# Kernel optimization log

Hardware: AMD Instinct MI355X
Metric: run time of the kernel (lower is better)

## Reference

```python
import jax, jax.numpy as jnp
import numpy as np

B, L, D, A, N, E, V, C = 16, 2048, 256, 128, 256, 50000, 30522, 128
H = D // 2  # GRU hidden per direction
EPS = 1e-5


def _rn(k, shape, s=0.02):
    return jax.random.normal(k, shape, jnp.float32) * s


def setup_inputs() -> dict:
    ks = jax.random.split(jax.random.key(0), 24)
    z = lambda *s: jnp.zeros(s, jnp.float32)
    return {
        "x": jax.random.randint(ks[0], (B, L), 0, V),
        "attention_mask": jnp.ones((B, L), jnp.float32),
        "nodes": jax.random.randint(ks[1], (B, N), 0, E),
        "node_mask": jnp.ones((B, N), jnp.float32),
        "D_D": jax.random.uniform(ks[2], (A, A), jnp.float32),
        "D_F": jax.random.uniform(ks[3], (B, A, N), jnp.float32),
        "word_embed": _rn(ks[4], (V, D)),
        "label_embed": _rn(ks[5], (A, D)),
        "entity_embed": _rn(ks[6], (E, D)),
        "W1": _rn(ks[7], (D, D)), "W2": _rn(ks[8], (D, D)),
        "W3": _rn(ks[9], (D, D)), "W4": _rn(ks[10], (D, D)),
        "W6_w": _rn(ks[11], (D, 2 * D)), "W6_b": z(D),
        "V1": _rn(ks[12], (D,), 1.0), "V2": _rn(ks[13], (D,), 1.0),
        "gru_wih_f": _rn(ks[14], (3 * H, D)), "gru_whh_f": _rn(ks[15], (3 * H, H)),
        "gru_bih_f": z(3 * H), "gru_bhh_f": z(3 * H),
        "gru_wih_b": _rn(ks[16], (3 * H, D)), "gru_whh_b": _rn(ks[17], (3 * H, H)),
        "gru_bih_b": z(3 * H), "gru_bhh_b": z(3 * H),
        "conv1_w": _rn(ks[18], (D, D, 3)), "conv1_b": z(D),
        "conv2_w": _rn(ks[19], (D, D, 4)), "conv2_b": z(D),
        "conv3_w": _rn(ks[20], (D, D, 5)), "conv3_b": z(D),
        "cls1_w": _rn(ks[21], (1024, 2 * D)), "cls1_b": z(1024),
        "cls2_w": _rn(ks[22], (C, 1024)), "cls2_b": z(C),
    }


def _gru_dir(x, wih, whh, bih, bhh, reverse):
    # x: [B,L,d] -> outputs [B,L,H]; torch GRU cell math
    gi = jnp.swapaxes(x, 0, 1) @ wih.T + bih  # [L,B,3H], input proj precomputed
    h0 = jnp.zeros((x.shape[0], whh.shape[1]), x.dtype)

    def step(h, g):
        gh = h @ whh.T + bhh
        ir, iz, inn = jnp.split(g, 3, -1)
        hr, hz, hn = jnp.split(gh, 3, -1)
        r = jax.nn.sigmoid(ir + hr)
        zt = jax.nn.sigmoid(iz + hz)
        n = jnp.tanh(inn + r * hn)
        hnew = (1.0 - zt) * n + zt * h
        return hnew, hnew

    _, hs = jax.lax.scan(step, h0, gi, reverse=reverse)
    return jnp.swapaxes(hs, 0, 1)


def _conv1d(x, w, b):
    # x: [B,C,L], w: [O,I,K], VALID padding (torch Conv1d default)
    y = jax.lax.conv_general_dilated(x, w, (1,), "VALID",
                                     dimension_numbers=("NCH", "OIH", "NCH"))
    return y + b[None, :, None]


def reference(x, attention_mask, nodes, node_mask, D_D, D_F, word_embed, label_embed,
              entity_embed, W1, W2, W3, W4, W6_w, W6_b, V1, V2,
              gru_wih_f, gru_whh_f, gru_bih_f, gru_bhh_f,
              gru_wih_b, gru_whh_b, gru_bih_b, gru_bhh_b,
              conv1_w, conv1_b, conv2_w, conv2_b, conv3_w, conv3_b,
              cls1_w, cls1_b, cls2_w, cls2_b):
    Dm = label_embed                                  # [A,d]
    Fm = entity_embed[nodes] * node_mask[..., None]   # [B,N,d]
    D_hat = jax.nn.relu(
        Dm @ W1.T
        + (D_D @ (Dm @ W2.T)) / (jnp.sum(D_D, 1, keepdims=True) + EPS)
        + (D_D.T @ (Dm @ W3.T)) / (jnp.sum(D_D.T, 1, keepdims=True) + EPS)
    )                                                 # [A,d]
    F_hat = jax.nn.relu(
        Fm @ W4.T
        + jnp.einsum("ban,ad->bnd", D_F, D_hat) / (jnp.sum(D_F, 1)[..., None] + EPS)
    ) * node_mask[..., None]                          # [B,N,d]

    xe = word_embed[x]                                # [B,L,d]
    hf = _gru_dir(xe, gru_wih_f, gru_whh_f, gru_bih_f, gru_bhh_f, False)
    hb = _gru_dir(xe, gru_wih_b, gru_whh_b, gru_bih_b, gru_bhh_b, True)
    H1 = jnp.mean(jnp.concatenate([hf, hb], -1), axis=1)  # [B,d]

    def attn_pool(feats, ctx, Vvec):
        cat = jnp.concatenate([feats, jnp.broadcast_to(ctx[:, None, :], feats.shape)], -1)
        U = jnp.tanh(cat @ W6_w.T + W6_b)             # [B,n,d]
        alpha = jax.nn.softmax(jnp.einsum("bnd,d->bn", U, Vvec), axis=1)
        return jnp.einsum("bn,bnd->bd", alpha, U)

    Hf = attn_pool(F_hat, H1, V1)                     # [B,d]
    xt = jnp.swapaxes(xe, 1, 2)                       # [B,d,L]
    Y = jnp.concatenate([
        jnp.swapaxes(_conv1d(xt, conv1_w, conv1_b), 1, 2),
        jnp.swapaxes(_conv1d(xt, conv2_w, conv2_b), 1, 2),
        jnp.swapaxes(_conv1d(xt, conv3_w, conv3_b), 1, 2),
    ], axis=1)                                        # [B,3L-12+3,d]
    Ht = attn_pool(Y, Hf, V2)                         # [B,d]
    Hcat = jnp.concatenate([Hf, Ht], -1)              # [B,2d]
    return jax.nn.relu(Hcat @ cls1_w.T + cls1_b) @ cls2_w.T + cls2_b
```

## Files before the change

kernel.cpp:

```cpp
#include <hip/hip_runtime.h>
#include <cstdint>
#include <cstddef>

constexpr int kB = 16, kL = 2048, kD = 256, kA = 128, kN = 256, kC = 128;
constexpr int kH = 128, kG = 384, kGN = 768;
constexpr int kT1 = 2046, kT2 = 2045, kT3 = 2044, kTT = 6135;
constexpr float kEPS = 1e-5f;

constexpr int kCTile = 48;
constexpr int kCBlkPerSeg = 43 * kB;
constexpr int kConvBlocks = 3 * kCBlkPerSeg;
constexpr int kGruBlocks = 32;

constexpr size_t OFF_XE   = 0;
constexpr size_t OFF_GI   = OFF_XE + (size_t)kB*kL*kD;
constexpr size_t OFF_FHAT = OFF_GI + (size_t)kB*kL*kGN;
constexpr size_t OFF_UF   = OFF_FHAT + (size_t)kB*kN*kD;
constexpr size_t OFF_EFFW = OFF_UF + (size_t)kB*kN*kD;
constexpr size_t OFF_EFFB = OFF_EFFW + (size_t)12*kD*kD;
constexpr size_t OFF_W6AT = OFF_EFFB + (size_t)3*kD;
constexpr size_t OFF_W6BT = OFF_W6AT + (size_t)kD*kD;
constexpr size_t OFF_W1T  = OFF_W6BT + (size_t)kD*kD;
constexpr size_t OFF_W2T  = OFF_W1T + (size_t)kD*kD;
constexpr size_t OFF_W3T  = OFF_W2T + (size_t)kD*kD;
constexpr size_t OFF_W4T  = OFF_W3T + (size_t)kD*kD;
constexpr size_t OFF_DHAT = OFF_W4T + (size_t)kD*kD;
constexpr size_t OFF_P1   = OFF_DHAT + (size_t)kA*kD;
constexpr size_t OFF_P2   = OFF_P1 + (size_t)kA*kD;
constexpr size_t OFF_P3   = OFF_P2 + (size_t)kA*kD;
constexpr size_t OFF_RS   = OFF_P3 + (size_t)kA*kD;
constexpr size_t OFF_CS   = OFF_RS + kA;
constexpr size_t OFF_H1   = OFF_CS + kA;
constexpr size_t OFF_C1   = OFF_H1 + (size_t)kB*kD;
constexpr size_t OFF_HFv  = OFF_C1 + (size_t)kB*kD;
constexpr size_t OFF_C2   = OFF_HFv + (size_t)kB*kD;
constexpr size_t OFF_HT   = OFF_C2 + (size_t)kB*kD;
constexpr size_t OFF_SCF  = OFF_HT + (size_t)kB*kD;
constexpr size_t OFF_SC   = OFF_SCF + (size_t)kB*kN;
constexpr size_t OFF_PART = OFF_SC + (size_t)kB*kTT;
constexpr size_t OFF_PBUF = OFF_PART + (size_t)48*kB*kD;
constexpr size_t TOTAL_CONCURRENT = OFF_PBUF + (size_t)kB*kTT*kD;

__device__ __forceinline__ float sigm(float x) { return 1.f / (1.f + __expf(-x)); }
__device__ __forceinline__ float tanh_fast(float x) {
  x = fminf(15.f, fmaxf(-15.f, x));
  float e2 = __expf(2.f * x);
  return (e2 - 1.f) / (e2 + 1.f);
}

__global__ void k_transpose(float* dst, const float* src, int stride) {
  int i = blockIdx.x, d = threadIdx.x;
  dst[i * kD + d] = src[(size_t)d * stride + i];
}

__global__ void k_rowcol(const float* DDm, float* rs, float* cs) {
  int a = threadIdx.x;
  float r = 0.f, c = 0.f;
  for (int j = 0; j < kA; ++j) { r += DDm[a * kA + j]; c += DDm[j * kA + a]; }
  rs[a] = r; cs[a] = c;
}

__global__ void k_proj3(const float* Dm, const float* W1T, const float* W2T, const float* W3T,
                        float* P1, float* P2, float* P3) {
  __shared__ float row[kD];
  int a = blockIdx.x, d = threadIdx.x;
  row[d] = Dm[a * kD + d];
  __syncthreads();
  float s1 = 0, s2 = 0, s3 = 0;
  for (int i = 0; i < kD; ++i) {
    float v = row[i];
    s1 = fmaf(v, W1T[i * kD + d], s1);
    s2 = fmaf(v, W2T[i * kD + d], s2);
    s3 = fmaf(v, W3T[i * kD + d], s3);
  }
  P1[a * kD + d] = s1; P2[a * kD + d] = s2; P3[a * kD + d] = s3;
}

__global__ void k_dhat(const float* DDm, const float* P1, const float* P2, const float* P3,
                       const float* rs, const float* cs, float* Dhat) {
  __shared__ float drow[kA], dcol[kA];
  int a = blockIdx.x, d = threadIdx.x;
  if (d < kA) { drow[d] = DDm[a * kA + d]; dcol[d] = DDm[d * kA + a]; }
  __syncthreads();
  float q2 = 0, q3 = 0;
  for (int j = 0; j < kA; ++j) {
    q2 = fmaf(drow[j], P2[j * kD + d], q2);
    q3 = fmaf(dcol[j], P3[j * kD + d], q3);
  }
  float v = P1[a * kD + d] + q2 / (rs[a] + kEPS) + q3 / (cs[a] + kEPS);
  Dhat[a * kD + d] = v > 0.f ? v : 0.f;
}

__global__ void k_fhat(const int* nodes, const float* nmask, const float* eemb,
                       const float* DF, const float* W4T, const float* Dhat, float* Fhat) {
  int b = blockIdx.y, n0 = blockIdx.x * 16, d = threadIdx.x;
  __shared__ float fm[16][kD];
  __shared__ float dc[kA][16];
  __shared__ float den[16], msk[16];
  for (int r = 0; r < 16; ++r) {
    int idx = nodes[b * kN + n0 + r];
    float m = nmask[b * kN + n0 + r];
    fm[r][d] = eemb[(size_t)idx * kD + d] * m;
    if (d == 0) msk[r] = m;
  }
  for (int q = 0; q < 8; ++q) {
    int e = q * 256 + d;
    int aa = e >> 4, nn = e & 15;
    dc[aa][nn] = DF[(size_t)b * kA * kN + (size_t)aa * kN + n0 + nn];
  }
  __syncthreads();
  if (d < 16) {
    float s = 0.f;
    for (int aa = 0; aa < kA; ++aa) s += dc[aa][d];
    den[d] = s;
  }
  __syncthreads();
  float a1[16], a2[16];
#pragma unroll
  for (int n = 0; n < 16; ++n) { a1[n] = 0.f; a2[n] = 0.f; }
  for (int i = 0; i < kD; ++i) {
    float w = W4T[i * kD + d];
#pragma unroll
    for (int n = 0; n < 16; ++n) a1[n] = fmaf(fm[n][i], w, a1[n]);
  }
  for (int aa = 0; aa < kA; ++aa) {
    float w = Dhat[aa * kD + d];
#pragma unroll
    for (int n = 0; n < 16; ++n) a2[n] = fmaf(dc[aa][n], w, a2[n]);
  }
#pragma unroll
  for (int n = 0; n < 16; ++n) {
    float v = a1[n] + a2[n] / (den[n] + kEPS);
    v = v > 0.f ? v : 0.f;
    Fhat[((size_t)b * kN + n0 + n) * kD + d] = v * msk[n];
  }
}

__global__ void k_xe(const int* x, const float* wemb, float* xe) {
  int r0 = blockIdx.x * 16;
  int t = threadIdx.x;
  int rr = t >> 6, c = t & 63;
  for (int s = 0; s < 4; ++s) {
    int r = r0 + rr + s * 4;
    int idx = x[r];
    ((float4*)(xe + (size_t)r * kD))[c] = ((const float4*)(wemb + (size_t)idx * kD))[c];
  }
}

__global__ __launch_bounds__(256) void k_gemm_gi(const float* Aa, const float* wf, const float* wb,
                                                 const float* bf, const float* bb, float* Cc) {
  __shared__ alignas(16) float As[64][68];
  __shared__ alignas(16) float Bs[64][68];
  int m0 = blockIdx.x * 64, n0 = blockIdx.y * 64;
  int tid = threadIdx.x;
  int tx = tid & 15, ty = tid >> 4;
  float acc[4][4];
#pragma unroll
  for (int q = 0; q < 4; ++q)
#pragma unroll
    for (int p = 0; p < 4; ++p) acc[q][p] = 0.f;
  for (int kk = 0; kk < 256; kk += 64) {
    {
      int r = tid >> 2, c0 = (tid & 3) * 16;
      const float* src = Aa + (size_t)(m0 + r) * kD + kk + c0;
      float4 v0 = ((const float4*)src)[0], v1 = ((const float4*)src)[1];
      float4 v2 = ((const float4*)src)[2], v3 = ((const float4*)src)[3];
      *((float4*)&As[r][c0])      = v0; *((float4*)&As[r][c0 + 4])  = v1;
      *((float4*)&As[r][c0 + 8])  = v2; *((float4*)&As[r][c0 + 12]) = v3;
      int n = n0 + r;
      const float* wsrc = (n < kG) ? (wf + (size_t)n * kD) : (wb + (size_t)(n - kG) * kD);
      wsrc += kk + c0;
      float4 w0 = ((const float4*)wsrc)[0], w1 = ((const float4*)wsrc)[1];
      float4 w2 = ((const float4*)wsrc)[2], w3 = ((const float4*)wsrc)[3];
      *((float4*)&Bs[r][c0])      = w0; *((float4*)&Bs[r][c0 + 4])  = w1;
      *((float4*)&Bs[r][c0 + 8])  = w2; *((float4*)&Bs[r][c0 + 12]) = w3;
    }
    __syncthreads();
#pragma unroll 4
    for (int k4 = 0; k4 < 16; ++k4) {
      float4 av[4], bv[4];
#pragma unroll
      for (int q = 0; q < 4; ++q) av[q] = *(const float4*)&As[ty * 4 + q][k4 * 4];
#pragma unroll
      for (int p = 0; p < 4; ++p) bv[p] = *(const float4*)&Bs[tx * 4 + p][k4 * 4];
#pragma unroll
      for (int q = 0; q < 4; ++q)
#pragma unroll
        for (int p = 0; p < 4; ++p) {
          acc[q][p] = fmaf(av[q].x, bv[p].x, acc[q][p]);
          acc[q][p] = fmaf(av[q].y, bv[p].y, acc[q][p]);
          acc[q][p] = fmaf(av[q].z, bv[p].z, acc[q][p]);
          acc[q][p] = fmaf(av[q].w, bv[p].w, acc[q][p]);
        }
    }
    __syncthreads();
  }
  int nbase = n0 + tx * 4;
  float bb4[4];
#pragma unroll
  for (int p = 0; p < 4; ++p) {
    int n = nbase + p;
    bb4[p] = (n < kG) ? bf[n] : bb[n - kG];
  }
#pragma unroll
  for (int q = 0; q < 4; ++q) {
    int m = m0 + ty * 4 + q;
    float4 o = make_float4(acc[q][0] + bb4[0], acc[q][1] + bb4[1],
                           acc[q][2] + bb4[2], acc[q][3] + bb4[3]);
    *((float4*)(Cc + (size_t)m * kGN + nbase)) = o;
  }
}

__device__ __forceinline__ int hpad(int i) { return (i >> 5) * 36 + (i & 31); }

__global__ __launch_bounds__(768, 3) void k_main(
    const float* __restrict__ gi, const float* __restrict__ whh_f, const float* __restrict__ whh_b,
    const float* __restrict__ bhh_f, const float* __restrict__ bhh_b, float* __restrict__ H1,
    const float* __restrict__ xe, const float* __restrict__ effW, const float* __restrict__ effB,
    float* __restrict__ P, int idOffset) {
  __shared__ alignas(16) float smem[(kCTile + 4) * kD];
  int id = blockIdx.x + idOffset;
  int tid = threadIdx.x;

  if (id < kGruBlocks) {
    int b = id >> 1, dir = id & 1;
    const float* whh = dir ? whh_b : whh_f;
    const float* bhh = dir ? bhh_b : bhh_f;
    float* h_sh = smem;
    float* gh   = smem + 144;

    int s = tid & 3;
    int g = tid >> 2;
    float w[2][32];
#pragma unroll
    for (int q = 0; q < 2; ++q) {
      const float4* wp = (const float4*)(whh + (size_t)(g * 2 + q) * kH + s * 32);
#pragma unroll
      for (int r = 0; r < 8; ++r) {
        float4 v = wp[r];
        w[q][4 * r] = v.x; w[q][4 * r + 1] = v.y; w[q][4 * r + 2] = v.z; w[q][4 * r + 3] = v.w;
      }
    }
    for (int i = tid; i < 144; i += 768) h_sh[i] = 0.f;

    float hreg = 0.f, hsum = 0.f;
    float bhr = 0.f, bhz = 0.f, bhn = 0.f;
    float ar = 0.f, az = 0.f, an = 0.f;
    float br = 0.f, bz = 0.f, bn = 0.f;
    const float* gib = gi + (size_t)b * kL * kGN + dir * kG + tid;
    if (tid < kH) {
      bhr = bhh[tid]; bhz = bhh[tid + kH]; bhn = bhh[tid + 2 * kH];
      const float* r0 = gib + (size_t)(dir ? (kL - 1) : 0) * kGN;
      const float* r1 = gib + (size_t)(dir ? (kL - 2) : 1) * kGN;
      ar = r0[0]; az = r0[kH]; an = r0[2 * kH];
      br = r1[0]; bz = r1[kH]; bn = r1[2 * kH];
    }
    __syncthreads();

#define GRU_STEP(cr, cz, cn, T)                                                   \
    {                                                                             \
      const float* hp = h_sh + s * 36;                                            \
      float4 h0 = *(const float4*)(hp + 0),  h1 = *(const float4*)(hp + 4);       \
      float4 h2 = *(const float4*)(hp + 8),  h3 = *(const float4*)(hp + 12);      \
      float4 h4 = *(const float4*)(hp + 16), h5 = *(const float4*)(hp + 20);      \
      float4 h6 = *(const float4*)(hp + 24), h7 = *(const float4*)(hp + 28);      \
      float a0 = 0.f, a1 = 0.f;                                                   \
      const float4 hv[8] = {h0, h1, h2, h3, h4, h5, h6, h7};                      \
      _Pragma("unroll")                                                           \
      for (int r = 0; r < 8; ++r) {                                               \
        float4 hh = hv[r];                                                        \
        a0 = fmaf(hh.x, w[0][4 * r], a0);     a1 = fmaf(hh.x, w[1][4 * r], a1);   \
        a0 = fmaf(hh.y, w[0][4 * r + 1], a0); a1 = fmaf(hh.y, w[1][4 * r + 1], a1);\
        a0 = fmaf(hh.z, w[0][4 * r + 2], a0); a1 = fmaf(hh.z, w[1][4 * r + 2], a1);\
        a0 = fmaf(hh.w, w[0][4 * r + 3], a0); a1 = fmaf(hh.w, w[1][4 * r + 3], a1);\
      }                                                                           \
      a0 += __shfl_xor(a0, 1); a0 += __shfl_xor(a0, 2);                           \
      a1 += __shfl_xor(a1, 1); a1 += __shfl_xor(a1, 2);                           \
      if (s == 0) { float2 o = make_float2(a0, a1); *(float2*)(gh + g * 2) = o; } \
      __syncthreads();                                                            \
      if (tid < kH) {                                                             \
        int tn = (T) + 2; if (tn > kL - 1) tn = kL - 1;                           \
        const float* gq = gib + (size_t)(dir ? (kL - 1 - tn) : tn) * kGN;         \
        float lr = gq[0], lz = gq[kH], ln = gq[2 * kH];                           \
        float hr = gh[tid] + bhr;                                                 \
        float hz = gh[tid + kH] + bhz;                                            \
        float hn = gh[tid + 2 * kH] + bhn;                                        \
        float rg = sigm(cr + hr);                                                 \
        float zg = sigm(cz + hz);                                                 \
        float ng = tanh_fast(cn + rg * hn);                                       \
        hreg = (1.f - zg) * ng + zg * hreg;                                       \
        hsum += hreg;                                                             \
        h_sh[hpad(tid)] = hreg;                                                   \
        cr = lr; cz = lz; cn = ln;                                                \
      }                                                                           \
      __syncthreads();                                                            \
    }

    for (int t = 0; t < kL; t += 2) {
      GRU_STEP(ar, az, an, t)
      GRU_STEP(br, bz, bn, t + 1)
    }
#undef GRU_STEP
    if (tid < kH) H1[b * kD + dir * kH + tid] = hsum * (1.f / (float)kL);

  } else {
    int cid = id - kGruBlocks;
    int seg = cid / kCBlkPerSeg;
    int rem = cid - seg * kCBlkPerSeg;
    int b = rem / 43;
    int tb = rem - b * 43;
    int t0 = tb * kCTile;
    int K = 3 + seg;
    int tapbase = (seg == 0) ? 0 : (seg == 1) ? 3 : 7;
    int Toff = (seg == 0) ? 0 : (seg == 1) ? kT1 : (kT1 + kT2);
    int Tk = (seg == 0) ? kT1 : (seg == 1) ? kT2 : kT3;

    float (*xl)[kD] = (float(*)[kD])smem;
    int nrow = kCTile + K - 1;
    {
      int total4 = nrow * 64;
      for (int gq = tid; gq < total4; gq += 768) {
        int r = gq >> 6, c4 = gq & 63;
        int row = t0 + r; if (row > kL - 1) row = kL - 1;
        ((float4*)&xl[r][0])[c4] = ((const float4*)(xe + ((size_t)b * kL + row) * kD))[c4];
      }
    }
    __syncthreads();

    int tx = tid & 63, tg = tid >> 6;
    int d0 = tx * 4;
    float acc[4][4];
#pragma unroll
    for (int tt = 0; tt < 4; ++tt)
#pragma unroll
      for (int q = 0; q < 4; ++q) acc[tt][q] = 0.f;
    for (int tap = 0; tap < K; ++tap) {
      const float* wq = effW + (size_t)(tapbase + tap) * kD * kD + d0;
      int rbase = tg * 4 + tap;
#pragma unroll 2
      for (int i = 0; i < kD; i += 4) {
        float4 xv[4];
#pragma unroll
        for (int tt = 0; tt < 4; ++tt) xv[tt] = *(const float4*)&xl[rbase + tt][i];
#pragma unroll
        for (int c = 0; c < 4; ++c) {
          float4 w4 = *(const float4*)(wq + (size_t)(i + c) * kD);
#pragma unroll
          for (int tt = 0; tt < 4; ++tt) {
            float xc = (c == 0) ? xv[tt].x : (c == 1) ? xv[tt].y : (c == 2) ? xv[tt].z : xv[tt].w;
            acc[tt][0] = fmaf(xc, w4.x, acc[tt][0]);
            acc[tt][1] = fmaf(xc, w4.y, acc[tt][1]);
            acc[tt][2] = fmaf(xc, w4.z, acc[tt][2]);
            acc[tt][3] = fmaf(xc, w4.w, acc[tt][3]);
          }
        }
      }
    }
    float4 eb = *(const float4*)(effB + seg * kD + d0);
#pragma unroll
    for (int tt = 0; tt < 4; ++tt) {
      int t = t0 + tg * 4 + tt;
      if (t < Tk) {
        float4 o = make_float4(acc[tt][0] + eb.x, acc[tt][1] + eb.y,
                               acc[tt][2] + eb.z, acc[tt][3] + eb.w);
        *((float4*)(P + ((size_t)b * kTT + Toff + t) * kD + d0)) = o;
      }
    }
  }
}

__global__ void k_ctxproj(const float* vec, const float* W6bT, const float* w6bias, float* out) {
  __shared__ float vrow[kD];
  int b = blockIdx.x, d = threadIdx.x;
  vrow[d] = vec[b * kD + d];
  __syncthreads();
  float acc = w6bias[d];
  for (int i = 0; i < kD; ++i) acc = fmaf(vrow[i], W6bT[i * kD + d], acc);
  out[b * kD + d] = acc;
}

__global__ void k_attn1(const float* Fhat, const float* W6aT, const float* c1,
                        const float* V1, float* UF, float* scF) {
  int b = blockIdx.y, n0 = blockIdx.x * 16, d = threadIdx.x;
  __shared__ float fr[16][kD];
  __shared__ float red[16][8];
  for (int r = 0; r < 16; ++r) fr[r][d] = Fhat[((size_t)b * kN + n0 + r) * kD + d];
  __syncthreads();
  float u[16];
#pragma unroll
  for (int n = 0; n < 16; ++n) u[n] = 0.f;
  for (int i = 0; i < kD; ++i) {
    float w = W6aT[i * kD + d];
#pragma unroll
    for (int n = 0; n < 16; ++n) u[n] = fmaf(fr[n][i], w, u[n]);
  }
  float cb = c1[b * kD + d];
  float v1 = V1[d];
  int lane = d & 63, wv = d >> 6;
#pragma unroll
  for (int n = 0; n < 16; ++n) {
    float uu = tanh_fast(u[n] + cb);
    UF[((size_t)b * kN + n0 + n) * kD + d] = uu;
    float p = uu * v1;
    p += __shfl_xor(p, 1); p += __shfl_xor(p, 2); p += __shfl_xor(p, 4);
    p += __shfl_xor(p, 8); p += __shfl_xor(p, 16); p += __shfl_xor(p, 32);
    if (lane == 0) red[n][wv] = p;
  }
  __syncthreads();
  if (d < 16) scF[b * kN + n0 + d] = red[d][0] + red[d][1] + red[d][2] + red[d][3];
}

__global__ void k_attn1_fin(const float* scF, const float* UF, float* Hf) {
  int b = blockIdx.x, d = threadIdx.x;
  __shared__ float al[kN];
  __shared__ float red[4];
  float sv = scF[b * kN + d];
  float m = sv;
#pragma unroll
  for (int o = 1; o < 64; o <<= 1) m = fmaxf(m, __shfl_xor(m, o));
  if ((d & 63) == 0) red[d >> 6] = m;
  __syncthreads();
  float mm = fmaxf(fmaxf(red[0], red[1]), fmaxf(red[2], red[3]));
  float e = __expf(sv - mm);
  float s = e;
#pragma unroll
  for (int o = 1; o < 64; o <<= 1) s += __shfl_xor(s, o);
  __syncthreads();
  if ((d & 63) == 0) red[d >> 6] = s;
  __syncthreads();
  float tot = red[0] + red[1] + red[2] + red[3];
  al[d] = e / tot;
  __syncthreads();
  float acc = 0.f;
  for (int n = 0; n < kN; ++n) acc = fmaf(al[n], UF[((size_t)b * kN + n) * kD + d], acc);
  Hf[b * kD + d] = acc;
}

__global__ void k_fold(const float* cw1, const float* cw2, const float* cw3,
                       const float* W6aT, float* effW) {
  int tapg = blockIdx.y, i0 = blockIdx.x * 4, d = threadIdx.x;
  const float* cw; int K, tap;
  if (tapg < 3)      { cw = cw1; K = 3; tap = tapg; }
  else if (tapg < 7) { cw = cw2; K = 4; tap = tapg - 3; }
  else               { cw = cw3; K = 5; tap = tapg - 7; }
  __shared__ float cc[4][kD];
#pragma unroll
  for (int ii = 0; ii < 4; ++ii)
    cc[ii][d] = cw[((size_t)d * kD + (i0 + ii)) * K + tap];
  __syncthreads();
  float acc[4] = {0.f, 0.f, 0.f, 0.f};
  for (int jj = 0; jj < kD; ++jj) {
    float w = W6aT[jj * kD + d];
#pragma unroll
    for (int ii = 0; ii < 4; ++ii) acc[ii] = fmaf(cc[ii][jj], w, acc[ii]);
  }
#pragma unroll
  for (int ii = 0; ii < 4; ++ii)
    effW[((size_t)tapg * kD + i0 + ii) * kD + d] = acc[ii];
}

__global__ void k_effb(const float* b1, const float* b2, const float* b3,
                       const float* W6aT, float* effB) {
  int c = blockIdx.x, d = threadIdx.x;
  const float* bb = (c == 0) ? b1 : ((c == 1) ? b2 : b3);
  __shared__ float bl[kD];
  bl[d] = bb[d];
  __syncthreads();
  float acc = 0.f;
  for (int j = 0; j < kD; ++j) acc = fmaf(bl[j], W6aT[j * kD + d], acc);
  effB[c * kD + d] = acc;
}

__global__ void k_score(const float* P, const float* c2, const float* V2, float* sc) {
  int b = blockIdx.y;
  int t0 = blockIdx.x * 32;
  int tid = threadIdx.x;
  int w = tid >> 6, lane = tid & 63;
  float4 c2v = ((const float4*)(c2 + (size_t)b * kD))[lane];
  float4 v2v = ((const float4*)V2)[lane];
#pragma unroll
  for (int it = 0; it < 8; ++it) {
    int t = t0 + it * 4 + w;
    if (t < kTT) {
      float4 p = ((const float4*)(P + ((size_t)b * kTT + t) * kD))[lane];
      float s = tanh_fast(p.x + c2v.x) * v2v.x + tanh_fast(p.y + c2v.y) * v2v.y +
                tanh_fast(p.z + c2v.z) * v2v.z + tanh_fast(p.w + c2v.w) * v2v.w;
      s += __shfl_xor(s, 1); s += __shfl_xor(s, 2); s += __shfl_xor(s, 4);
      s += __shfl_xor(s, 8); s += __shfl_xor(s, 16); s += __shfl_xor(s, 32);
      if (lane == 0) sc[(size_t)b * kTT + t] = s;
    }
  }
}

__global__ void k_sm2(float* sc) {
  int b = blockIdx.x, tid = threadIdx.x;
  __shared__ float red[4];
  float m = -1e30f;
  for (int t = tid; t < kTT; t += 256) m = fmaxf(m, sc[(size_t)b * kTT + t]);
#pragma unroll
  for (int o = 1; o < 64; o <<= 1) m = fmaxf(m, __shfl_xor(m, o));
  if ((tid & 63) == 0) red[tid >> 6] = m;
  __syncthreads();
  float mm = fmaxf(fmaxf(red[0], red[1]), fmaxf(red[2], red[3]));
  float s = 0.f;
  for (int t = tid; t < kTT; t += 256) s += __expf(sc[(size_t)b * kTT + t] - mm);
#pragma unroll
  for (int o = 1; o < 64; o <<= 1) s += __shfl_xor(s, o);
  __syncthreads();
  if ((tid & 63) == 0) red[tid >> 6] = s;
  __syncthreads();
  float inv = 1.f / (red[0] + red[1] + red[2] + red[3]);
  for (int t = tid; t < kTT; t += 256) sc[(size_t)b * kTT + t] = __expf(sc[(size_t)b * kTT + t] - mm) * inv;
}

__global__ void k_aws(const float* sc, const float* P, const float* c2, float* part) {
  int cchunk = blockIdx.x, b = blockIdx.y, d = threadIdx.x;
  int tbeg = cchunk * 128;
  int tend = tbeg + 128; if (tend > kTT) tend = kTT;
  float c2d = c2[(size_t)b * kD + d];
  float acc = 0.f;
  for (int t = tbeg; t < tend; ++t)
    acc = fmaf(sc[(size_t)b * kTT + t], tanh_fast(P[((size_t)b * kTT + t) * kD + d] + c2d), acc);
  part[((size_t)cchunk * kB + b) * kD + d] = acc;
}

__global__ void k_ared(const float* part, float* Ht) {
  int b = blockIdx.x, d = threadIdx.x;
  float acc = 0.f;
  for (int cc = 0; cc < 48; ++cc) acc += part[((size_t)cc * kB + b) * kD + d];
  Ht[b * kD + d] = acc;
}

__global__ __launch_bounds__(1024) void k_cls(const float* Hf, const float* Ht,
                                              const float* w1, const float* b1,
                                              const float* w2, const float* b2, float* out) {
  int b = blockIdx.x, tid = threadIdx.x;
  __shared__ alignas(16) float hc[2 * kD];
  __shared__ alignas(16) float act[1024];
  if (tid < kD) hc[tid] = Hf[b * kD + tid];
  else if (tid < 2 * kD) hc[tid] = Ht[b * kD + tid - kD];
  __syncthreads();
  {
    float acc = b1[tid];
    const float4* wr = (const float4*)(w1 + (size_t)tid * 2 * kD);
    const float4* hr = (const float4*)hc;
    for (int i = 0; i < 128; ++i) {
      float4 wv = wr[i]; float4 hv = hr[i];
      acc += wv.x * hv.x + wv.y * hv.y + wv.z * hv.z + wv.w * hv.w;
    }
    act[tid] = acc > 0.f ? acc : 0.f;
  }
  __syncthreads();
  if (tid < kC) {
    float acc = b2[tid];
    const float4* wr = (const float4*)(w2 + (size_t)tid * 1024);
    const float4* ar = (const float4*)act;
    for (int i = 0; i < 256; ++i) {
      float4 wv = wr[i]; float4 av = ar[i];
      acc += wv.x * av.x + wv.y * av.y + wv.z * av.z + wv.w * av.w;
    }
    out[b * kC + tid] = acc;
  }
}

extern "C" void kernel_launch(void* const* d_in, const int* in_sizes, int n_in,
                              void* d_out, int out_size, void* d_ws, size_t ws_size,
                              hipStream_t stream) {
  (void)in_sizes; (void)n_in; (void)out_size;
  const int*   x     = (const int*)d_in[0];
  const int*   nodes = (const int*)d_in[2];
  const float* nmask = (const float*)d_in[3];
  const float* DDm   = (const float*)d_in[4];
  const float* DF    = (const float*)d_in[5];
  const float* wemb  = (const float*)d_in[6];
  const float* lemb  = (const float*)d_in[7];
  const float* eemb  = (const float*)d_in[8];
  const float* W1    = (const float*)d_in[9];
  const float* W2    = (const float*)d_in[10];
  const float* W3    = (const float*)d_in[11];
  const float* W4    = (const float*)d_in[12];
  const float* W6w   = (const float*)d_in[13];
  const float* W6bia = (const float*)d_in[14];
  const float* V1v   = (const float*)d_in[15];
  const float* V2v   = (const float*)d_in[16];
  const float* wih_f = (const float*)d_in[17];
  const float* whh_f = (const float*)d_in[18];
  const float* bih_f = (const float*)d_in[19];
  const float* bhh_f = (const float*)d_in[20];
  const float* wih_b = (const float*)d_in[21];
  const float* whh_b = (const float*)d_in[22];
  const float* bih_b = (const float*)d_in[23];
  const float* bhh_b = (const float*)d_in[24];
  const float* c1w   = (const float*)d_in[25];
  const float* c1b   = (const float*)d_in[26];
  const float* c2w   = (const float*)d_in[27];
  const float* c2b   = (const float*)d_in[28];
  const float* c3w   = (const float*)d_in[29];
  const float* c3b   = (const float*)d_in[30];
  const float* cls1w = (const float*)d_in[31];
  const float* cls1b = (const float*)d_in[32];
  const float* cls2w = (const float*)d_in[33];
  const float* cls2b = (const float*)d_in[34];
  float* out = (float*)d_out;
  float* ws  = (float*)d_ws;

  float* xe   = ws + OFF_XE;
  float* gi   = ws + OFF_GI;
  float* Fhat = ws + OFF_FHAT;
  float* UF   = ws + OFF_UF;
  float* effW = ws + OFF_EFFW;
  float* effB = ws + OFF_EFFB;
  float* w6at = ws + OFF_W6AT;
  float* w6bt = ws + OFF_W6BT;
  float* w1t  = ws + OFF_W1T;
  float* w2t  = ws + OFF_W2T;
  float* w3t  = ws + OFF_W3T;
  float* w4t  = ws + OFF_W4T;
  float* dhat = ws + OFF_DHAT;
  float* p1   = ws + OFF_P1;
  float* p2   = ws + OFF_P2;
  float* p3   = ws + OFF_P3;
  float* rs   = ws + OFF_RS;
  float* cs   = ws + OFF_CS;
  float* H1b  = ws + OFF_H1;
  float* c1bf = ws + OFF_C1;
  float* Hfb  = ws + OFF_HFv;
  float* c2bf = ws + OFF_C2;
  float* Htb  = ws + OFF_HT;
  float* scF  = ws + OFF_SCF;
  float* sc   = ws + OFF_SC;
  float* part = ws + OFF_PART;

  bool concurrent = ws_size >= TOTAL_CONCURRENT * sizeof(float);
  float* Pbuf = concurrent ? (ws + OFF_PBUF) : gi;

  k_xe<<<2048, 256, 0, stream>>>(x, wemb, xe);
  k_transpose<<<kD, kD, 0, stream>>>(w1t, W1, kD);
  k_transpose<<<kD, kD, 0, stream>>>(w2t, W2, kD);
  k_transpose<<<kD, kD, 0, stream>>>(w3t, W3, kD);
  k_transpose<<<kD, kD, 0, stream>>>(w4t, W4, kD);
  k_transpose<<<kD, kD, 0, stream>>>(w6at, W6w, 2 * kD);
  k_transpose<<<kD, kD, 0, stream>>>(w6bt, W6w + kD, 2 * kD);
  k_gemm_gi<<<dim3(512, 12), 256, 0, stream>>>(xe, wih_f, wih_b, bih_f, bih_b, gi);

  k_rowcol<<<1, kA, 0, stream>>>(DDm, rs, cs);
  k_proj3<<<kA, kD, 0, stream>>>(lemb, w1t, w2t, w3t, p1, p2, p3);
  k_dhat<<<kA, kD, 0, stream>>>(DDm, p1, p2, p3, rs, cs, dhat);
  k_fhat<<<dim3(16, kB), kD, 0, stream>>>(nodes, nmask, eemb, DF, w4t, dhat, Fhat);

  k_fold<<<dim3(64, 12), kD, 0, stream>>>(c1w, c2w, c3w, w6at, effW);
  k_effb<<<3, kD, 0, stream>>>(c1b, c2b, c3b, w6at, effB);

  if (concurrent) {
    k_main<<<kGruBlocks + kConvBlocks, 768, 0, stream>>>(
        gi, whh_f, whh_b, bhh_f, bhh_b, H1b, xe, effW, effB, Pbuf, 0);
  } else {
    k_main<<<kGruBlocks, 768, 0, stream>>>(
        gi, whh_f, whh_b, bhh_f, bhh_b, H1b, xe, effW, effB, Pbuf, 0);
    k_main<<<kConvBlocks, 768, 0, stream>>>(
        gi, whh_f, whh_b, bhh_f, bhh_b, H1b, xe, effW, effB, Pbuf, kGruBlocks);
  }

  k_ctxproj<<<kB, kD, 0, stream>>>(H1b, w6bt, W6bia, c1bf);
  k_attn1<<<dim3(16, kB), kD, 0, stream>>>(Fhat, w6at, c1bf, V1v, UF, scF);
  k_attn1_fin<<<kB, kD, 0, stream>>>(scF, UF, Hfb);
  k_ctxproj<<<kB, kD, 0, stream>>>(Hfb, w6bt, W6bia, c2bf);

  k_score<<<dim3(192, kB), 256, 0, stream>>>(Pbuf, c2bf, V2v, sc);
  k_sm2<<<kB, 256, 0, stream>>>(sc);
  k_aws<<<dim3(48, kB), kD, 0, stream>>>(sc, Pbuf, c2bf, part);
  k_ared<<<kB, kD, 0, stream>>>(part, Htb);
  k_cls<<<kB, 1024, 0, stream>>>(Hfb, Htb, cls1w, cls1b, cls2w, cls2b, out);
}
```

Measured before the change: 2.197 ms.

## Restructure GRU recurrence to 1024 threads with one barrier per step

The GRU recurrence in the fused main kernel now runs with 1024 threads. Each group of 8 lanes owns one hidden unit and computes all three gate dot products, reducing them with DPP lane swizzles instead of shuffles. The kernel double-buffers h in shared memory so each step needs a single barrier rather than two, and input-projection rows for 8 future steps are staged into shared memory in chunks instead of loaded per step. The conv path is adapted to 1024 threads with 3 time rows per thread group. This targets the serial latency per GRU step, at the cost of more threads per block and different register and occupancy pressure in the conv blocks.

```diff
diff --git a/kernel.cpp b/kernel.cpp
--- a/kernel.cpp
+++ b/kernel.cpp
@@ -11,6 +11,10 @@
 constexpr int kCBlkPerSeg = 43 * kB;
 constexpr int kConvBlocks = 3 * kCBlkPerSeg;
 constexpr int kGruBlocks = 32;
+
+constexpr int kSmemFloats = 21504;
+
+typedef float f32x4 __attribute__((ext_vector_type(4)));
 
 constexpr size_t OFF_XE   = 0;
 constexpr size_t OFF_GI   = OFF_XE + (size_t)kB*kL*kD;
@@ -48,6 +52,19 @@
   return (e2 - 1.f) / (e2 + 1.f);
 }
 
+__device__ __forceinline__ float dpp_xor1(float x) {
+  int r = __builtin_amdgcn_update_dpp(0, __builtin_bit_cast(int, x), 0xB1, 0xF, 0xF, true);
+  return __builtin_bit_cast(float, r);
+}
+__device__ __forceinline__ float dpp_xor2(float x) {
+  int r = __builtin_amdgcn_update_dpp(0, __builtin_bit_cast(int, x), 0x4E, 0xF, 0xF, true);
+  return __builtin_bit_cast(float, r);
+}
+__device__ __forceinline__ float dpp_mirr8(float x) {
+  int r = __builtin_amdgcn_update_dpp(0, __builtin_bit_cast(int, x), 0x141, 0xF, 0xF, true);
+  return __builtin_bit_cast(float, r);
+}
+
 __global__ void k_transpose(float* dst, const float* src, int stride) {
   int i = blockIdx.x, d = threadIdx.x;
   dst[i * kD + d] = src[(size_t)d * stride + i];
@@ -211,14 +228,15 @@
   }
 }
 
-__device__ __forceinline__ int hpad(int i) { return (i >> 5) * 36 + (i & 31); }
-
-__global__ __launch_bounds__(768, 3) void k_main(
+__global__
+__attribute__((amdgpu_flat_work_group_size(1024, 1024)))
+__attribute__((amdgpu_waves_per_eu(4, 4)))
+void k_main(
     const float* __restrict__ gi, const float* __restrict__ whh_f, const float* __restrict__ whh_b,
     const float* __restrict__ bhh_f, const float* __restrict__ bhh_b, float* __restrict__ H1,
     const float* __restrict__ xe, const float* __restrict__ effW, const float* __restrict__ effB,
     float* __restrict__ P, int idOffset) {
-  __shared__ alignas(16) float smem[(kCTile + 4) * kD];
+  __shared__ alignas(16) float smem[kSmemFloats];
   int id = blockIdx.x + idOffset;
   int tid = threadIdx.x;
 
@@ -226,82 +244,83 @@
     int b = id >> 1, dir = id & 1;
     const float* whh = dir ? whh_b : whh_f;
     const float* bhh = dir ? bhh_b : bhh_f;
-    float* h_sh = smem;
-    float* gh   = smem + 144;
-
-    int s = tid & 3;
-    int g = tid >> 2;
-    float w[2][32];
-#pragma unroll
-    for (int q = 0; q < 2; ++q) {
-      const float4* wp = (const float4*)(whh + (size_t)(g * 2 + q) * kH + s * 32);
-#pragma unroll
-      for (int r = 0; r < 8; ++r) {
-        float4 v = wp[r];
-        w[q][4 * r] = v.x; w[q][4 * r + 1] = v.y; w[q][4 * r + 2] = v.z; w[q][4 * r + 3] = v.w;
-      }
-    }
-    for (int i = tid; i < 144; i += 768) h_sh[i] = 0.f;
-
-    float hreg = 0.f, hsum = 0.f;
-    float bhr = 0.f, bhz = 0.f, bhn = 0.f;
-    float ar = 0.f, az = 0.f, an = 0.f;
-    float br = 0.f, bz = 0.f, bn = 0.f;
-    const float* gib = gi + (size_t)b * kL * kGN + dir * kG + tid;
-    if (tid < kH) {
-      bhr = bhh[tid]; bhz = bhh[tid + kH]; bhn = bhh[tid + 2 * kH];
-      const float* r0 = gib + (size_t)(dir ? (kL - 1) : 0) * kGN;
-      const float* r1 = gib + (size_t)(dir ? (kL - 2) : 1) * kGN;
-      ar = r0[0]; az = r0[kH]; an = r0[2 * kH];
-      br = r1[0]; bz = r1[kH]; bn = r1[2 * kH];
-    }
+    float* hb = smem;
+    float* gt = smem + 320;
+
+    int i = tid >> 3, q = tid & 7;
+    int hpad_i = i + ((i >> 4) << 2);
+
+    const f32x4* wrp = (const f32x4*)(whh + (size_t)i * kH + q * 16);
+    const f32x4* wzp = (const f32x4*)(whh + (size_t)(kH + i) * kH + q * 16);
+    const f32x4* wnp = (const f32x4*)(whh + (size_t)(2 * kH + i) * kH + q * 16);
+    f32x4 wr0 = wrp[0], wr1 = wrp[1], wr2 = wrp[2], wr3 = wrp[3];
+    f32x4 wz0 = wzp[0], wz1 = wzp[1], wz2 = wzp[2], wz3 = wzp[3];
+    f32x4 wn0 = wnp[0], wn1 = wnp[1], wn2 = wnp[2], wn3 = wnp[3];
+
+    float bhr = bhh[i], bhz = bhh[kH + i], bhn = bhh[2 * kH + i];
+
+    const float* gibase = gi + (size_t)b * kL * kGN + dir * kG;
+    float va, vb, vc;
+
+#define STAGE_LOAD(T)                                                          \
+    { int o0 = tid / 384, c0 = tid - o0 * 384;                                 \
+      int r0 = dir ? (kL - 1 - ((T) + o0)) : ((T) + o0);                       \
+      r0 = r0 < 0 ? 0 : (r0 > kL - 1 ? kL - 1 : r0);                           \
+      va = gibase[(size_t)r0 * kGN + c0];                                      \
+      int u1 = tid + 1024; int o1 = u1 / 384, c1 = u1 - o1 * 384;              \
+      int r1 = dir ? (kL - 1 - ((T) + o1)) : ((T) + o1);                       \
+      r1 = r1 < 0 ? 0 : (r1 > kL - 1 ? kL - 1 : r1);                           \
+      vb = gibase[(size_t)r1 * kGN + c1];                                      \
+      int u2 = tid + 2048; int o2 = u2 / 384, c2 = u2 - o2 * 384;              \
+      int r2 = dir ? (kL - 1 - ((T) + o2)) : ((T) + o2);                       \
+      r2 = r2 < 0 ? 0 : (r2 > kL - 1 ? kL - 1 : r2);                           \
+      vc = gibase[(size_t)r2 * kGN + c2]; }
+
+#define STAGE_WRITE(cbuf)                                                      \
+    { gt[(cbuf) * 3072 + tid] = va;                                            \
+      gt[(cbuf) * 3072 + tid + 1024] = vb;                                     \
+      gt[(cbuf) * 3072 + tid + 2048] = vc; }
+
+    for (int u = tid; u < 320; u += 1024) hb[u] = 0.f;
+    STAGE_LOAD(0)
+    STAGE_WRITE(0)
+    float hprev = 0.f, hsum = 0.f;
     __syncthreads();
 
-#define GRU_STEP(cr, cz, cn, T)                                                   \
-    {                                                                             \
-      const float* hp = h_sh + s * 36;                                            \
-      float4 h0 = *(const float4*)(hp + 0),  h1 = *(const float4*)(hp + 4);       \
-      float4 h2 = *(const float4*)(hp + 8),  h3 = *(const float4*)(hp + 12);      \
-      float4 h4 = *(const float4*)(hp + 16), h5 = *(const float4*)(hp + 20);      \
-      float4 h6 = *(const float4*)(hp + 24), h7 = *(const float4*)(hp + 28);      \
-      float a0 = 0.f, a1 = 0.f;                                                   \
-      const float4 hv[8] = {h0, h1, h2, h3, h4, h5, h6, h7};                      \
-      _Pragma("unroll")                                                           \
-      for (int r = 0; r < 8; ++r) {                                               \
-        float4 hh = hv[r];                                                        \
-        a0 = fmaf(hh.x, w[0][4 * r], a0);     a1 = fmaf(hh.x, w[1][4 * r], a1);   \
-        a0 = fmaf(hh.y, w[0][4 * r + 1], a0); a1 = fmaf(hh.y, w[1][4 * r + 1], a1);\
-        a0 = fmaf(hh.z, w[0][4 * r + 2], a0); a1 = fmaf(hh.z, w[1][4 * r + 2], a1);\
-        a0 = fmaf(hh.w, w[0][4 * r + 3], a0); a1 = fmaf(hh.w, w[1][4 * r + 3], a1);\
-      }                                                                           \
-      a0 += __shfl_xor(a0, 1); a0 += __shfl_xor(a0, 2);                           \
-      a1 += __shfl_xor(a1, 1); a1 += __shfl_xor(a1, 2);                           \
-      if (s == 0) { float2 o = make_float2(a0, a1); *(float2*)(gh + g * 2) = o; } \
-      __syncthreads();                                                            \
-      if (tid < kH) {                                                             \
-        int tn = (T) + 2; if (tn > kL - 1) tn = kL - 1;                           \
-        const float* gq = gib + (size_t)(dir ? (kL - 1 - tn) : tn) * kGN;         \
-        float lr = gq[0], lz = gq[kH], ln = gq[2 * kH];                           \
-        float hr = gh[tid] + bhr;                                                 \
-        float hz = gh[tid + kH] + bhz;                                            \
-        float hn = gh[tid + 2 * kH] + bhn;                                        \
-        float rg = sigm(cr + hr);                                                 \
-        float zg = sigm(cz + hz);                                                 \
-        float ng = tanh_fast(cn + rg * hn);                                       \
-        hreg = (1.f - zg) * ng + zg * hreg;                                       \
-        hsum += hreg;                                                             \
-        h_sh[hpad(tid)] = hreg;                                                   \
-        cr = lr; cz = lz; cn = ln;                                                \
-      }                                                                           \
-      __syncthreads();                                                            \
-    }
-
-    for (int t = 0; t < kL; t += 2) {
-      GRU_STEP(ar, az, an, t)
-      GRU_STEP(br, bz, bn, t + 1)
-    }
-#undef GRU_STEP
-    if (tid < kH) H1[b * kD + dir * kH + tid] = hsum * (1.f / (float)kL);
+#define FMA_Q(hq, wrq, wzq, wnq)                                               \
+    ar = fmaf(hq.x, wrq.x, ar); az = fmaf(hq.x, wzq.x, az); an = fmaf(hq.x, wnq.x, an); \
+    ar = fmaf(hq.y, wrq.y, ar); az = fmaf(hq.y, wzq.y, az); an = fmaf(hq.y, wnq.y, an); \
+    ar = fmaf(hq.z, wrq.z, ar); az = fmaf(hq.z, wzq.z, az); an = fmaf(hq.z, wnq.z, an); \
+    ar = fmaf(hq.w, wrq.w, ar); az = fmaf(hq.w, wzq.w, az); an = fmaf(hq.w, wnq.w, an);
+
+    for (int t = 0; t < kL; ++t) {
+      int cb = (t >> 3) & 1;
+      if ((t & 7) == 0 && t + 8 < kL) STAGE_LOAD(t + 8)
+      const f32x4* hp = (const f32x4*)(hb + (t & 1) * 160 + q * 20);
+      f32x4 h0 = hp[0], h1 = hp[1], h2 = hp[2], h3 = hp[3];
+      float ar = 0.f, az = 0.f, an = 0.f;
+      FMA_Q(h0, wr0, wz0, wn0)
+      FMA_Q(h1, wr1, wz1, wn1)
+      FMA_Q(h2, wr2, wz2, wn2)
+      FMA_Q(h3, wr3, wz3, wn3)
+      ar += dpp_xor1(ar); az += dpp_xor1(az); an += dpp_xor1(an);
+      ar += dpp_xor2(ar); az += dpp_xor2(az); an += dpp_xor2(an);
+      ar += dpp_mirr8(ar); az += dpp_mirr8(az); an += dpp_mirr8(an);
+      int gb = cb * 3072 + (t & 7) * 384 + i;
+      float gir = gt[gb], giz = gt[gb + kH], gin = gt[gb + 2 * kH];
+      float rr = sigm(gir + ar + bhr);
+      float zz = sigm(giz + az + bhz);
+      float nn = tanh_fast(gin + rr * (an + bhn));
+      hprev = (1.f - zz) * nn + zz * hprev;
+      hsum += hprev;
+      if (q == 0) hb[((t + 1) & 1) * 160 + hpad_i] = hprev;
+      if ((t & 7) == 7 && t + 1 < kL) STAGE_WRITE(cb ^ 1)
+      __syncthreads();
+    }
+#undef FMA_Q
+#undef STAGE_LOAD
+#undef STAGE_WRITE
+    if (q == 0) H1[b * kD + dir * kH + i] = hsum * (1.f / (float)kL);
 
   } else {
     int cid = id - kGruBlocks;
@@ -319,7 +338,7 @@
     int nrow = kCTile + K - 1;
     {
       int total4 = nrow * 64;
-      for (int gq = tid; gq < total4; gq += 768) {
+      for (int gq = tid; gq < total4; gq += 1024) {
         int r = gq >> 6, c4 = gq & 63;
         int row = t0 + r; if (row > kL - 1) row = kL - 1;
         ((float4*)&xl[r][0])[c4] = ((const float4*)(xe + ((size_t)b * kL + row) * kD))[c4];
@@ -329,24 +348,24 @@
 
     int tx = tid & 63, tg = tid >> 6;
     int d0 = tx * 4;
-    float acc[4][4];
-#pragma unroll
-    for (int tt = 0; tt < 4; ++tt)
-#pragma unroll
-      for (int q = 0; q < 4; ++q) acc[tt][q] = 0.f;
+    float acc[3][4];
+#pragma unroll
+    for (int tt = 0; tt < 3; ++tt)
+#pragma unroll
+      for (int qq = 0; qq < 4; ++qq) acc[tt][qq] = 0.f;
     for (int tap = 0; tap < K; ++tap) {
       const float* wq = effW + (size_t)(tapbase + tap) * kD * kD + d0;
-      int rbase = tg * 4 + tap;
+      int rbase = tg * 3 + tap;
 #pragma unroll 2
-      for (int i = 0; i < kD; i += 4) {
-        float4 xv[4];
-#pragma unroll
-        for (int tt = 0; tt < 4; ++tt) xv[tt] = *(const float4*)&xl[rbase + tt][i];
+      for (int ii = 0; ii < kD; ii += 4) {
+        float4 xv[3];
+#pragma unroll
+        for (int tt = 0; tt < 3; ++tt) xv[tt] = *(const float4*)&xl[rbase + tt][ii];
 #pragma unroll
         for (int c = 0; c < 4; ++c) {
-          float4 w4 = *(const float4*)(wq + (size_t)(i + c) * kD);
-#pragma unroll
-          for (int tt = 0; tt < 4; ++tt) {
+          float4 w4 = *(const float4*)(wq + (size_t)(ii + c) * kD);
+#pragma unroll
+          for (int tt = 0; tt < 3; ++tt) {
             float xc = (c == 0) ? xv[tt].x : (c == 1) ? xv[tt].y : (c == 2) ? xv[tt].z : xv[tt].w;
             acc[tt][0] = fmaf(xc, w4.x, acc[tt][0]);
             acc[tt][1] = fmaf(xc, w4.y, acc[tt][1]);
@@ -358,8 +377,8 @@
     }
     float4 eb = *(const float4*)(effB + seg * kD + d0);
 #pragma unroll
-    for (int tt = 0; tt < 4; ++tt) {
-      int t = t0 + tg * 4 + tt;
+    for (int tt = 0; tt < 3; ++tt) {
+      int t = t0 + tg * 3 + tt;
       if (t < Tk) {
         float4 o = make_float4(acc[tt][0] + eb.x, acc[tt][1] + eb.y,
                                acc[tt][2] + eb.z, acc[tt][3] + eb.w);
@@ -652,12 +671,12 @@
   k_effb<<<3, kD, 0, stream>>>(c1b, c2b, c3b, w6at, effB);
 
   if (concurrent) {
-    k_main<<<kGruBlocks + kConvBlocks, 768, 0, stream>>>(
+    k_main<<<kGruBlocks + kConvBlocks, 1024, 0, stream>>>(
         gi, whh_f, whh_b, bhh_f, bhh_b, H1b, xe, effW, effB, Pbuf, 0);
   } else {
-    k_main<<<kGruBlocks, 768, 0, stream>>>(
+    k_main<<<kGruBlocks, 1024, 0, stream>>>(
         gi, whh_f, whh_b, bhh_f, bhh_b, H1b, xe, effW, effB, Pbuf, 0);
-    k_main<<<kConvBlocks, 768, 0, stream>>>(
+    k_main<<<kConvBlocks, 1024, 0, stream>>>(
         gi, whh_f, whh_b, bhh_f, bhh_b, H1b, xe, effW, effB, Pbuf, kGruBlocks);
   }
 
```

New measurement: 2.443 ms. 11.2% more time.
